# Optimization experiments

Hardware: AMD Instinct MI355X
Metric: run time of the kernel (lower is better)

The kernel has to match this reference:

```python
import jax, jax.numpy as jnp
import numpy as np

HIDDEN_DIM = 256
NLAT, NLON = 64, 128
BATCH, N_STATIONS = 2, 1024


def _grid_coords():
    lat = jnp.linspace(-90.0, 90.0, NLAT)
    lon = jnp.linspace(-180.0, 180.0, NLON)
    lat_mesh, lon_mesh = jnp.meshgrid(lat, lon, indexing='ij')
    return lat_mesh.reshape(-1), lon_mesh.reshape(-1)  # (n_grid,)


def setup_inputs() -> dict:
    key = jax.random.key(0)
    k1, k2, k3, k4, k5, k6 = jax.random.split(key, 6)
    station_features = jax.random.normal(k1, (BATCH, N_STATIONS, HIDDEN_DIM), dtype=jnp.float32)
    station_coords = jax.random.normal(k2, (BATCH, N_STATIONS, 3), dtype=jnp.float32)
    mask = jnp.ones((BATCH, N_STATIONS), dtype=jnp.float32)
    # distance_mlp params: Linear(3,32) -> GELU -> Linear(32,1) -> Softplus
    W1 = jax.random.normal(k3, (3, 32), dtype=jnp.float32) * (1.0 / np.sqrt(3.0))
    b1 = jax.random.normal(k4, (32,), dtype=jnp.float32) * 0.02
    W2 = jax.random.normal(k5, (32, 1), dtype=jnp.float32) * (1.0 / np.sqrt(32.0))
    b2 = jax.random.normal(k6, (1,), dtype=jnp.float32) * 0.02
    return {"station_features": station_features, "station_coords": station_coords,
            "mask": mask, "W1": W1, "b1": b1, "W2": W2, "b2": b2}


def reference(station_features, station_coords, mask, W1, b1, W2, b2):
    lat_grid, lon_grid = _grid_coords()  # (G,)
    station_lat = station_coords[:, :, 0]  # (B,S)
    station_lon = station_coords[:, :, 1]
    dlat = station_lat[:, :, None] - lat_grid[None, None, :]  # (B,S,G)
    dlon = station_lon[:, :, None] - lon_grid[None, None, :]
    dist = jnp.sqrt(dlat**2 + dlon**2 + 1e-6)
    dist_features = jnp.stack([dist, dlat, dlon], axis=-1)  # (B,S,G,3)
    h = jax.nn.gelu(dist_features @ W1 + b1, approximate=False)  # (B,S,G,32)
    weights = jax.nn.softplus((h @ W2 + b2)[..., 0])  # (B,S,G)
    weights = weights * mask[:, :, None]
    weights = jax.nn.softmax(weights, axis=1)  # over stations
    grid = jnp.einsum('bsg,bsd->bgd', weights, station_features)
    grid = grid.reshape(station_features.shape[0], NLAT, NLON, HIDDEN_DIM)
    return jnp.transpose(grid, (0, 3, 1, 2))  # (B, D, nlat, nlon)
```

## Files before the change

### kernel.cpp

```cpp
#include <hip/hip_runtime.h>
#include <math.h>

#define NLAT 64
#define NLON 128
#define HID  256
#define NSTA 1024
#define TG   16
#define SC   128
#define NCHUNK (NSTA / SC)
#define NGRP 16
#define TABN 4096
#define TABW 4.5f

#define LOG2E 1.4426950408889634f
#define LN2   0.69314718055994531f

typedef float f32x4 __attribute__((ext_vector_type(4)));
typedef _Float16 f16x8 __attribute__((ext_vector_type(8)));
typedef _Float16 f16x4 __attribute__((ext_vector_type(4)));

__device__ __forceinline__ float gelu_ref(float x) {
    const float p  = 0.3275911f;
    const float a1 = 0.254829592f, a2 = -0.284496736f, a3 = 1.421413741f,
                a4 = -1.453152027f, a5 = 1.061405429f;
    float z  = x * 0.70710678118654752f;
    float az = fabsf(z);
    float t  = __builtin_amdgcn_rcpf(fmaf(p, az, 1.0f));
    float poly = fmaf(fmaf(fmaf(fmaf(a5, t, a4), t, a3), t, a2), t, a1) * t;
    float e  = __builtin_amdgcn_exp2f(az * az * -LOG2E);
    float r  = fmaf(-poly, e, 1.0f);
    float erfz = copysignf(r, z);
    float hx = 0.5f * x;
    return fmaf(hx, erfz, hx);
}

__global__ __launch_bounds__(256)
void cvt_kernel(const float* __restrict__ feats, _Float16* __restrict__ fhi,
                _Float16* __restrict__ flo) {
    __shared__ float tile[16][64];
    const int blk = blockIdx.x;
    const int b  = blk >> 8;
    const int st = (blk >> 2) & 63;
    const int dt = blk & 3;
    {
        const int s  = threadIdx.x >> 4;
        const int dq = threadIdx.x & 15;
        const float4 vv = *(const float4*)
            &feats[((size_t)(b * NSTA + st * 16 + s)) * HID + dt * 64 + dq * 4];
        *(float4*)&tile[s][dq * 4] = vv;
    }
    __syncthreads();
    const int d  = threadIdx.x >> 2;
    const int sq = threadIdx.x & 3;
    f16x4 hi4, lo4;
#pragma unroll
    for (int k = 0; k < 4; ++k) {
        float v = tile[sq * 4 + k][d];
        _Float16 h = (_Float16)v;
        hi4[k] = h;
        lo4[k] = (_Float16)(v - (float)h);
    }
    const size_t o = ((size_t)(b * HID + dt * 64 + d)) * NSTA + st * 16 + sq * 4;
    *(f16x4*)&fhi[o] = hi4;
    *(f16x4*)&flo[o] = lo4;
}

__global__ __launch_bounds__(256, 4)
void s2g_kernel(const float* __restrict__ coords,
                const float* __restrict__ maskp,
                const float* __restrict__ W1,
                const float* __restrict__ b1,
                const float* __restrict__ W2,
                const float* __restrict__ b2p,
                const _Float16* __restrict__ fhi,
                const _Float16* __restrict__ flo,
                float* __restrict__ out)
{
    __shared__ float gtab[TABN];
    __shared__ __align__(16) f16x8 fragAh[256];
    __shared__ __align__(16) f16x8 fragAl[256];
    __shared__ __align__(16) float slat[SC], slon[SC], smask[SC];
    __shared__ float4 wpack[32];
    __shared__ float w2s[32];
    __shared__ __align__(16) float maxbuf[NGRP * TG], psum[NGRP * TG];
    __shared__ __align__(16) float mS[TG], lS[TG], alphaS[TG];

    const int tid  = threadIdx.x;
    const int blk  = blockIdx.x & 511;
    const int b    = blockIdx.x >> 9;
    const int lat  = blk >> 3;
    const int lon0 = (blk & 7) * TG;

    const float latv = -90.0f + (180.0f / 63.0f) * (float)lat;

    const float TH = 2.0f * TABW / (float)TABN;
#pragma unroll
    for (int k = tid; k < TABN; k += 256) {
        float x = -TABW + ((float)k + 0.5f) * TH;
        gtab[k] = gelu_ref(x) - fmaxf(x, 0.0f);
    }
    if (tid < 32) {
        wpack[tid] = make_float4(W1[tid], W1[32 + tid], W1[64 + tid], b1[tid]);
        w2s[tid]   = W2[tid];
        if (tid < TG) { mS[tid] = -1.0e30f; lS[tid] = 0.0f; }
    }
    const float b2 = b2p[0];

    const int gA   = tid & (TG - 1);
    const int sgrp = tid >> 4;
    const float lonvA = -180.0f + (360.0f / 127.0f) * (float)(lon0 + gA);

    const int lane = tid & 63;
    const int wv   = tid >> 6;

    f32x4 acc[4];
#pragma unroll
    for (int t = 0; t < 4; ++t) acc[t] = (f32x4){0.0f, 0.0f, 0.0f, 0.0f};

    const float* cbase = coords + (size_t)b * NSTA * 3;
    const float* mbase = maskp  + (size_t)b * NSTA;
    const _Float16* fhb = fhi + (size_t)b * HID * NSTA;
    const _Float16* flb = flo + (size_t)b * HID * NSTA;

    const float ISCALE = (float)TABN / (2.0f * TABW);
    const float IOFF   = (float)TABN * 0.5f;

    for (int c = 0; c < NCHUNK; ++c) {
        const int s0 = c * SC;
        __syncthreads();
        if (tid < SC) {
            slat[tid]  = cbase[(size_t)(s0 + tid) * 3 + 0];
            slon[tid]  = cbase[(size_t)(s0 + tid) * 3 + 1];
            smask[tid] = mbase[s0 + tid];
        }
        __syncthreads();

        float dist[8], dlat[8], dlon[8], v[8];
#pragma unroll
        for (int i = 0; i < 8; ++i) {
            int s = sgrp * 8 + i;
            float dla = slat[s] - latv;
            float dlo = slon[s] - lonvA;
            dlat[i] = dla;
            dlon[i] = dlo;
            dist[i] = sqrtf(fmaf(dla, dla, fmaf(dlo, dlo, 1e-6f)));
            v[i] = b2;
        }
#pragma unroll 2
        for (int j = 0; j < 32; ++j) {
            float4 wj = wpack[j];
            float  w2 = w2s[j];
#pragma unroll
            for (int i = 0; i < 8; ++i) {
                float pre = fmaf(wj.x, dist[i], fmaf(wj.y, dlat[i], fmaf(wj.z, dlon[i], wj.w)));
                float cl  = fminf(fmaxf(pre, -TABW), 4.4999f);
                int  idx  = (int)fmaf(cl, ISCALE, IOFF);
                float r   = gtab[idx];
                v[i] = fmaf(w2, fmaxf(pre, 0.0f), v[i]);
                v[i] = fmaf(w2, r, v[i]);
            }
        }
        float lmax = -3.0e38f;
#pragma unroll
        for (int i = 0; i < 8; ++i) {
            int s = sgrp * 8 + i;
            float x  = v[i];
            float ax = fabsf(x);
            float e  = __builtin_amdgcn_exp2f(-ax * LOG2E);
            float sp = fmaxf(x, 0.0f) + __builtin_amdgcn_logf(1.0f + e) * LN2;
            v[i] = sp * smask[s];
            lmax = fmaxf(lmax, v[i]);
        }
        maxbuf[sgrp * TG + gA] = lmax;
        __syncthreads();

        if (tid < TG) {
            float cm = maxbuf[tid];
#pragma unroll
            for (int k = 1; k < NGRP; ++k) cm = fmaxf(cm, maxbuf[k * TG + tid]);
            float mold = mS[tid];
            float mnew = fmaxf(mold, cm);
            alphaS[tid] = __builtin_amdgcn_exp2f((mold - mnew) * LOG2E);
            mS[tid] = mnew;
        }
        __syncthreads();

        {
            float m  = mS[gA];
            float ps = 0.0f;
            f16x8 fh, fl;
#pragma unroll
            for (int i = 0; i < 8; ++i) {
                float p = __builtin_amdgcn_exp2f((v[i] - m) * LOG2E);
                _Float16 h = (_Float16)p;
                fh[i] = h;
                fl[i] = (_Float16)(p - (float)h);
                ps += p;
            }
            const int idx = ((sgrp >> 2) << 6) + (((sgrp & 3) << 4) | gA);
            fragAh[idx] = fh;
            fragAl[idx] = fl;
            psum[sgrp * TG + gA] = ps;
        }
        __syncthreads();

        if (tid < TG) {
            float t = 0.0f;
#pragma unroll
            for (int k = 0; k < NGRP; ++k) t += psum[k * TG + tid];
            lS[tid] = lS[tid] * alphaS[tid] + t;
        }

        {
            const f32x4 al = *(const f32x4*)&alphaS[(lane >> 4) * 4];
#pragma unroll
            for (int t = 0; t < 4; ++t) acc[t] = acc[t] * al;

            const int srow = s0 + ((lane >> 4) * 8);
            const int dbase = wv * 64 + (lane & 15);
#pragma unroll
            for (int kc = 0; kc < 4; ++kc) {
                f16x8 ah = fragAh[(kc << 6) + lane];
                f16x8 al16 = fragAl[(kc << 6) + lane];
#pragma unroll
                for (int t = 0; t < 4; ++t) {
                    const size_t off = (size_t)(dbase + t * 16) * NSTA + srow + kc * 32;
                    f16x8 bh = *(const f16x8*)(fhb + off);
                    f16x8 bl = *(const f16x8*)(flb + off);
                    acc[t] = __builtin_amdgcn_mfma_f32_16x16x32_f16(ah, bh, acc[t], 0, 0, 0);
                    acc[t] = __builtin_amdgcn_mfma_f32_16x16x32_f16(ah, bl, acc[t], 0, 0, 0);
                    acc[t] = __builtin_amdgcn_mfma_f32_16x16x32_f16(al16, bh, acc[t], 0, 0, 0);
                }
            }
        }
    }
    __syncthreads();

    {
        const float4 l4 = *(const float4*)&lS[(lane >> 4) * 4];
        const float4 rl = make_float4(1.0f / l4.x, 1.0f / l4.y, 1.0f / l4.z, 1.0f / l4.w);
        const int m0 = (lane >> 4) * 4;
        const size_t gbase = (size_t)lat * NLON + lon0 + m0;
#pragma unroll
        for (int t = 0; t < 4; ++t) {
            const int d = wv * 64 + t * 16 + (lane & 15);
            float4 o;
            o.x = acc[t].x * rl.x;
            o.y = acc[t].y * rl.y;
            o.z = acc[t].z * rl.z;
            o.w = acc[t].w * rl.w;
            *reinterpret_cast<float4*>(out + ((size_t)(b * HID + d)) * (NLAT * NLON) + gbase) = o;
        }
    }
}

extern "C" void kernel_launch(void* const* d_in, const int* in_sizes, int n_in,
                              void* d_out, int out_size, void* d_ws, size_t ws_size,
                              hipStream_t stream) {
    const float* feats  = (const float*)d_in[0];
    const float* coords = (const float*)d_in[1];
    const float* maskp  = (const float*)d_in[2];
    const float* W1     = (const float*)d_in[3];
    const float* b1     = (const float*)d_in[4];
    const float* W2     = (const float*)d_in[5];
    const float* b2     = (const float*)d_in[6];
    float* out          = (float*)d_out;

    _Float16* fhi = (_Float16*)d_ws;
    _Float16* flo = fhi + (size_t)2 * HID * NSTA;

    hipLaunchKernelGGL(cvt_kernel, dim3(512), dim3(256), 0, stream, feats, fhi, flo);
    hipLaunchKernelGGL(s2g_kernel, dim3(1024), dim3(256), 0, stream,
                       coords, maskp, W1, b1, W2, b2, fhi, flo, out);
}
```

Before: 252.1 us.

## Split station reduction across two blocks and merge partial softmax sums

Each grid tile's online-softmax over stations is split into two halves handled by separate blocks, which doubles the grid to 2048 blocks. Each half writes unnormalised partial accumulators plus its (max, sum) pair to workspace, and a new combine kernel merges them with log-sum-exp rescaling. The GELU lookup table now uses a symmetric half-range table with pre-scaled W1 weights to save index arithmetic and shared memory, and occupancy hints rise to 8 blocks per CU. The conversion kernel processes 32 stations per block with padded tiles. The cost is extra global traffic for a second 16 MB accumulator plus the read-modify-write combine pass.

```diff
diff --git a/kernel.cpp b/kernel.cpp
--- a/kernel.cpp
+++ b/kernel.cpp
@@ -5,11 +5,12 @@
 #define NLON 128
 #define HID  256
 #define NSTA 1024
+#define NG   (NLAT * NLON)
 #define TG   16
 #define SC   128
-#define NCHUNK (NSTA / SC)
+#define NCH  4
 #define NGRP 16
-#define TABN 4096
+#define TABN 2048
 #define TABW 4.5f
 
 #define LOG2E 1.4426950408889634f
@@ -17,7 +18,6 @@
 
 typedef float f32x4 __attribute__((ext_vector_type(4)));
 typedef _Float16 f16x8 __attribute__((ext_vector_type(8)));
-typedef _Float16 f16x4 __attribute__((ext_vector_type(4)));
 
 __device__ __forceinline__ float gelu_ref(float x) {
     const float p  = 0.3275911f;
@@ -37,35 +37,37 @@
 __global__ __launch_bounds__(256)
 void cvt_kernel(const float* __restrict__ feats, _Float16* __restrict__ fhi,
                 _Float16* __restrict__ flo) {
-    __shared__ float tile[16][64];
+    __shared__ float tile[32][68];
     const int blk = blockIdx.x;
-    const int b  = blk >> 8;
-    const int st = (blk >> 2) & 63;
+    const int b  = blk >> 7;
+    const int st = (blk >> 2) & 31;
     const int dt = blk & 3;
     {
-        const int s  = threadIdx.x >> 4;
-        const int dq = threadIdx.x & 15;
-        const float4 vv = *(const float4*)
-            &feats[((size_t)(b * NSTA + st * 16 + s)) * HID + dt * 64 + dq * 4];
-        *(float4*)&tile[s][dq * 4] = vv;
+        const int s  = threadIdx.x >> 3;
+        const int dq = threadIdx.x & 7;
+        const float* src = feats + ((size_t)(b * NSTA + st * 32 + s)) * HID + dt * 64 + dq * 8;
+        float4 v0 = *(const float4*)src;
+        float4 v1 = *(const float4*)(src + 4);
+        *(float4*)&tile[s][dq * 8]     = v0;
+        *(float4*)&tile[s][dq * 8 + 4] = v1;
     }
     __syncthreads();
     const int d  = threadIdx.x >> 2;
     const int sq = threadIdx.x & 3;
-    f16x4 hi4, lo4;
-#pragma unroll
-    for (int k = 0; k < 4; ++k) {
-        float v = tile[sq * 4 + k][d];
+    f16x8 hi8, lo8;
+#pragma unroll
+    for (int k = 0; k < 8; ++k) {
+        float v = tile[sq * 8 + k][d];
         _Float16 h = (_Float16)v;
-        hi4[k] = h;
-        lo4[k] = (_Float16)(v - (float)h);
-    }
-    const size_t o = ((size_t)(b * HID + dt * 64 + d)) * NSTA + st * 16 + sq * 4;
-    *(f16x4*)&fhi[o] = hi4;
-    *(f16x4*)&flo[o] = lo4;
-}
-
-__global__ __launch_bounds__(256, 4)
+        hi8[k] = h;
+        lo8[k] = (_Float16)(v - (float)h);
+    }
+    const size_t o = ((size_t)(b * HID + dt * 64 + d)) * NSTA + st * 32 + sq * 8;
+    *(f16x8*)&fhi[o] = hi8;
+    *(f16x8*)&flo[o] = lo8;
+}
+
+__global__ __launch_bounds__(256, 8)
 void s2g_kernel(const float* __restrict__ coords,
                 const float* __restrict__ maskp,
                 const float* __restrict__ W1,
@@ -74,34 +76,41 @@
                 const float* __restrict__ b2p,
                 const _Float16* __restrict__ fhi,
                 const _Float16* __restrict__ flo,
-                float* __restrict__ out)
+                float* __restrict__ out,
+                float* __restrict__ acc1,
+                float2* __restrict__ ml)
 {
     __shared__ float gtab[TABN];
     __shared__ __align__(16) f16x8 fragAh[256];
     __shared__ __align__(16) f16x8 fragAl[256];
     __shared__ __align__(16) float slat[SC], slon[SC], smask[SC];
     __shared__ float4 wpack[32];
-    __shared__ float w2s[32];
-    __shared__ __align__(16) float maxbuf[NGRP * TG], psum[NGRP * TG];
+    __shared__ float2 w2pk[32];
+    __shared__ __align__(16) float redbuf[NGRP * TG];
     __shared__ __align__(16) float mS[TG], lS[TG], alphaS[TG];
 
     const int tid  = threadIdx.x;
+    const int half = blockIdx.x >> 10;
+    const int b    = (blockIdx.x >> 9) & 1;
     const int blk  = blockIdx.x & 511;
-    const int b    = blockIdx.x >> 9;
     const int lat  = blk >> 3;
     const int lon0 = (blk & 7) * TG;
+    const int sbase = half * (NSTA / 2);
 
     const float latv = -90.0f + (180.0f / 63.0f) * (float)lat;
 
-    const float TH = 2.0f * TABW / (float)TABN;
+    const float CELL   = TABW / (float)TABN;
+    const float ISCALE = (float)TABN / TABW;
+
 #pragma unroll
     for (int k = tid; k < TABN; k += 256) {
-        float x = -TABW + ((float)k + 0.5f) * TH;
-        gtab[k] = gelu_ref(x) - fmaxf(x, 0.0f);
+        float x = ((float)k + 0.5f) * CELL;
+        gtab[k] = gelu_ref(-x);
     }
     if (tid < 32) {
-        wpack[tid] = make_float4(W1[tid], W1[32 + tid], W1[64 + tid], b1[tid]);
-        w2s[tid]   = W2[tid];
+        wpack[tid] = make_float4(W1[tid] * ISCALE, W1[32 + tid] * ISCALE,
+                                 W1[64 + tid] * ISCALE, b1[tid] * ISCALE);
+        w2pk[tid]  = make_float2(W2[tid], W2[tid] * CELL);
         if (tid < TG) { mS[tid] = -1.0e30f; lS[tid] = 0.0f; }
     }
     const float b2 = b2p[0];
@@ -122,11 +131,8 @@
     const _Float16* fhb = fhi + (size_t)b * HID * NSTA;
     const _Float16* flb = flo + (size_t)b * HID * NSTA;
 
-    const float ISCALE = (float)TABN / (2.0f * TABW);
-    const float IOFF   = (float)TABN * 0.5f;
-
-    for (int c = 0; c < NCHUNK; ++c) {
-        const int s0 = c * SC;
+    for (int c = 0; c < NCH; ++c) {
+        const int s0 = sbase + c * SC;
         __syncthreads();
         if (tid < SC) {
             slat[tid]  = cbase[(size_t)(s0 + tid) * 3 + 0];
@@ -149,15 +155,15 @@
 #pragma unroll 2
         for (int j = 0; j < 32; ++j) {
             float4 wj = wpack[j];
-            float  w2 = w2s[j];
+            float2 w2 = w2pk[j];
 #pragma unroll
             for (int i = 0; i < 8; ++i) {
                 float pre = fmaf(wj.x, dist[i], fmaf(wj.y, dlat[i], fmaf(wj.z, dlon[i], wj.w)));
-                float cl  = fminf(fmaxf(pre, -TABW), 4.4999f);
-                int  idx  = (int)fmaf(cl, ISCALE, IOFF);
+                float a   = fminf(fabsf(pre), (float)TABN - 0.5f);
+                int  idx  = (int)a;
                 float r   = gtab[idx];
-                v[i] = fmaf(w2, fmaxf(pre, 0.0f), v[i]);
-                v[i] = fmaf(w2, r, v[i]);
+                v[i] = fmaf(w2.y, fmaxf(pre, 0.0f), v[i]);
+                v[i] = fmaf(w2.x, r, v[i]);
             }
         }
         float lmax = -3.0e38f;
@@ -171,13 +177,13 @@
             v[i] = sp * smask[s];
             lmax = fmaxf(lmax, v[i]);
         }
-        maxbuf[sgrp * TG + gA] = lmax;
+        redbuf[sgrp * TG + gA] = lmax;
         __syncthreads();
 
         if (tid < TG) {
-            float cm = maxbuf[tid];
-#pragma unroll
-            for (int k = 1; k < NGRP; ++k) cm = fmaxf(cm, maxbuf[k * TG + tid]);
+            float cm = redbuf[tid];
+#pragma unroll
+            for (int k = 1; k < NGRP; ++k) cm = fmaxf(cm, redbuf[k * TG + tid]);
             float mold = mS[tid];
             float mnew = fmaxf(mold, cm);
             alphaS[tid] = __builtin_amdgcn_exp2f((mold - mnew) * LOG2E);
@@ -200,14 +206,14 @@
             const int idx = ((sgrp >> 2) << 6) + (((sgrp & 3) << 4) | gA);
             fragAh[idx] = fh;
             fragAl[idx] = fl;
-            psum[sgrp * TG + gA] = ps;
+            redbuf[sgrp * TG + gA] = ps;
         }
         __syncthreads();
 
         if (tid < TG) {
             float t = 0.0f;
 #pragma unroll
-            for (int k = 0; k < NGRP; ++k) t += psum[k * TG + tid];
+            for (int k = 0; k < NGRP; ++k) t += redbuf[k * TG + tid];
             lS[tid] = lS[tid] * alphaS[tid] + t;
         }
 
@@ -237,20 +243,43 @@
     __syncthreads();
 
     {
-        const float4 l4 = *(const float4*)&lS[(lane >> 4) * 4];
-        const float4 rl = make_float4(1.0f / l4.x, 1.0f / l4.y, 1.0f / l4.z, 1.0f / l4.w);
+        float* dst = half ? acc1 : out;
         const int m0 = (lane >> 4) * 4;
         const size_t gbase = (size_t)lat * NLON + lon0 + m0;
 #pragma unroll
         for (int t = 0; t < 4; ++t) {
             const int d = wv * 64 + t * 16 + (lane & 15);
-            float4 o;
-            o.x = acc[t].x * rl.x;
-            o.y = acc[t].y * rl.y;
-            o.z = acc[t].z * rl.z;
-            o.w = acc[t].w * rl.w;
-            *reinterpret_cast<float4*>(out + ((size_t)(b * HID + d)) * (NLAT * NLON) + gbase) = o;
-        }
+            *reinterpret_cast<f32x4*>(dst + ((size_t)(b * HID + d)) * NG + gbase) = acc[t];
+        }
+        if (tid < TG)
+            ml[((half << 1) + b) * NG + lat * NLON + lon0 + tid] = make_float2(mS[tid], lS[tid]);
+    }
+}
+
+__global__ __launch_bounds__(256)
+void comb_kernel(float* __restrict__ out, const float* __restrict__ acc1,
+                 const float2* __restrict__ ml) {
+    const int x    = blockIdx.x;
+    const int b    = x >> 9;
+    const int lat  = (x >> 3) & 63;
+    const int dseg = x & 7;
+    const int lon  = threadIdx.x & 127;
+    const int dsub = threadIdx.x >> 7;
+    const int g    = lat * NLON + lon;
+
+    const float2 p0 = ml[b * NG + g];
+    const float2 p1 = ml[(2 + b) * NG + g];
+    const float M  = fmaxf(p0.x, p1.x);
+    float s0 = __builtin_amdgcn_exp2f((p0.x - M) * LOG2E);
+    float s1 = __builtin_amdgcn_exp2f((p1.x - M) * LOG2E);
+    const float rl = 1.0f / fmaf(p0.y, s0, p1.y * s1);
+    s0 *= rl; s1 *= rl;
+
+#pragma unroll 4
+    for (int k = 0; k < 16; ++k) {
+        const int d = dseg * 32 + dsub + k * 2;
+        const size_t o = ((size_t)(b * HID + d)) * NG + g;
+        out[o] = fmaf(out[o], s0, acc1[o] * s1);
     }
 }
 
@@ -268,8 +297,11 @@
 
     _Float16* fhi = (_Float16*)d_ws;
     _Float16* flo = fhi + (size_t)2 * HID * NSTA;
-
-    hipLaunchKernelGGL(cvt_kernel, dim3(512), dim3(256), 0, stream, feats, fhi, flo);
-    hipLaunchKernelGGL(s2g_kernel, dim3(1024), dim3(256), 0, stream,
-                       coords, maskp, W1, b1, W2, b2, fhi, flo, out);
-}
+    float*  acc1 = (float*)((char*)d_ws + (size_t)2 * 1048576);
+    float2* ml   = (float2*)((char*)d_ws + (size_t)2 * 1048576 + (size_t)2 * HID * NG * 4);
+
+    hipLaunchKernelGGL(cvt_kernel, dim3(256), dim3(256), 0, stream, feats, fhi, flo);
+    hipLaunchKernelGGL(s2g_kernel, dim3(2048), dim3(256), 0, stream,
+                       coords, maskp, W1, b1, W2, b2, fhi, flo, out, acc1, ml);
+    hipLaunchKernelGGL(comb_kernel, dim3(1024), dim3(256), 0, stream, out, acc1, ml);
+}
```

Measured after the change: 268.5 us. +6.5%, slower.
